# Kernel tuning notes

Measured on AMD Instinct MI355X. Metric: run time of the kernel, lower is better.

The kernel has to match this reference:

```python
import jax, jax.numpy as jnp
import numpy as np

B, N, D, U = 8, 2048, 512, 128


def setup_inputs() -> dict:
    key = jax.random.key(0)
    k_x, k_q, k_k, k_v, k_o = jax.random.split(key, 5)
    scale_in = 1.0 / np.sqrt(D)
    scale_u = 1.0 / np.sqrt(U)
    return {
        "inputs": jax.random.normal(k_x, (B, N, D), dtype=jnp.float32),
        "W_q": jax.random.normal(k_q, (D, U), dtype=jnp.float32) * scale_in,
        "W_k": jax.random.normal(k_k, (D, U), dtype=jnp.float32) * scale_in,
        "W_v": jax.random.normal(k_v, (D, U), dtype=jnp.float32) * scale_in,
        "W_o": jax.random.normal(k_o, (U, D), dtype=jnp.float32) * scale_u,
        "b_o": jnp.zeros((D,), dtype=jnp.float32),
    }


def reference(inputs, W_q, W_k, W_v, W_o, b_o):
    # Single-head scaled dot-product self-attention + output dense + residual
    Q = jnp.einsum('bnd,du->bnu', inputs, W_q)
    K = jnp.einsum('bnd,du->bnu', inputs, W_k)
    V = jnp.einsum('bnd,du->bnu', inputs, W_v)
    inv_sqrt_u = 1.0 / jnp.sqrt(jnp.asarray(W_q.shape[-1], inputs.dtype))
    scores = jnp.einsum('bnu,bmu->bnm', Q, K) * inv_sqrt_u  # [B,N,N]
    attn = jax.nn.softmax(scores, axis=-1)
    ctx = jnp.einsum('bnm,bmu->bnu', attn, V)  # [B,N,U]
    return jnp.einsum('bnu,ud->bnd', ctx, W_o) + b_o + inputs
```

## Files before the change

### kernel.cpp

```cpp
#include <hip/hip_runtime.h>

#define BB 8
#define NN 2048
#define DD 512
#define UU 128
#define SPLITS 8
#define KSPLIT 256
#define TK 32

typedef __bf16 bf16_t;
typedef __bf16 bf16x4 __attribute__((ext_vector_type(4)));
typedef __bf16 bf16x8 __attribute__((ext_vector_type(8)));
typedef float floatx4 __attribute__((ext_vector_type(4)));

__device__ __forceinline__ floatx4 mfma16(bf16x8 a, bf16x8 b, floatx4 c) {
  return __builtin_amdgcn_mfma_f32_16x16x32_bf16(a, b, c, 0, 0, 0);
}

#define SW(r, g) ((((g) ^ ((r) & 7)) * 8))

__device__ __forceinline__ void gld_lds16(const bf16_t* g, bf16_t* l) {
  __builtin_amdgcn_global_load_lds(
      (const __attribute__((address_space(1))) unsigned int*)g,
      (__attribute__((address_space(3))) unsigned int*)l, 16, 0, 0);
}

__global__ __launch_bounds__(256) void cast_x_kernel(const float* __restrict__ x,
                                                     bf16_t* __restrict__ xb) {
  int G = blockIdx.x * 256 + threadIdx.x;
  int token = G >> 6;
  int g = G & 63;
  int dstg = (g & 56) | ((g & 7) ^ (token & 7));
  const float4* src = reinterpret_cast<const float4*>(x) + (size_t)G * 2;
  float4 a = src[0], b = src[1];
  bf16x8 o;
  o[0] = (bf16_t)a.x; o[1] = (bf16_t)a.y; o[2] = (bf16_t)a.z; o[3] = (bf16_t)a.w;
  o[4] = (bf16_t)b.x; o[5] = (bf16_t)b.y; o[6] = (bf16_t)b.z; o[7] = (bf16_t)b.w;
  *reinterpret_cast<bf16x8*>(&xb[(size_t)token * 512 + dstg * 8]) = o;
}

__global__ __launch_bounds__(256) void pack_w_kernel(const float* __restrict__ wq,
                                                     const float* __restrict__ wk,
                                                     const float* __restrict__ wv,
                                                     const float* __restrict__ wo,
                                                     bf16_t* __restrict__ wqkvt,
                                                     bf16_t* __restrict__ wot) {
  int gid = blockIdx.x * 256 + threadIdx.x;
  if (gid < 384 * 512) {
    int nrow = gid >> 9;
    int kdst = gid & 511;
    int ksrc = (kdst & ~56) | (((((kdst >> 3) & 7)) ^ (nrow & 7)) << 3);
    const float* src = (nrow < 128) ? wq : ((nrow < 256) ? wk : wv);
    int n = nrow & 127;
    wqkvt[gid] = (bf16_t)src[ksrc * 128 + n];
  } else {
    int g = gid - 384 * 512;
    int nrow = g >> 7;
    int kdst = g & 127;
    int ksrc = (kdst & ~56) | (((((kdst >> 3) & 7)) ^ (nrow & 7)) << 3);
    wot[g] = (bf16_t)wo[ksrc * 512 + nrow];
  }
}

__global__ __launch_bounds__(256, 2) void qkv_gemm_kernel(const bf16_t* __restrict__ xb,
                                                          const bf16_t* __restrict__ wqkvt,
                                                          bf16_t* __restrict__ Q,
                                                          bf16_t* __restrict__ K,
                                                          bf16_t* __restrict__ Vt) {
  __shared__ bf16_t lA[128 * 64];
  __shared__ bf16_t lB[128 * 64];
  const int m0 = blockIdx.x * 128;
  const int n0 = blockIdx.y * 128;
  const int tid = threadIdx.x;
  const int w = tid >> 6, lane = tid & 63;
  const int quad = lane >> 4, l15 = lane & 15;
  const int mh = (w & 1) * 64, nh = (w >> 1) * 64;

  floatx4 zero4 = {0.f, 0.f, 0.f, 0.f};
  floatx4 acc[4][4];
#pragma unroll
  for (int mt = 0; mt < 4; mt++)
#pragma unroll
    for (int nt = 0; nt < 4; nt++) acc[mt][nt] = zero4;

  for (int kc = 0; kc < 512; kc += 64) {
    __syncthreads();
#pragma unroll
    for (int i = 0; i < 4; i++) {
      int G = tid + i * 256;
      int r = G >> 3, g = G & 7;
      gld_lds16(&xb[(size_t)(m0 + r) * 512 + kc + g * 8], &lA[G * 8]);
    }
#pragma unroll
    for (int i = 0; i < 4; i++) {
      int G = tid + i * 256;
      int r = G >> 3, g = G & 7;
      gld_lds16(&wqkvt[(size_t)(n0 + r) * 512 + kc + g * 8], &lB[G * 8]);
    }
    asm volatile("s_waitcnt vmcnt(0)" ::: "memory");
    __syncthreads();
#pragma unroll
    for (int kb = 0; kb < 2; kb++) {
      bf16x8 af[4], bfr[4];
#pragma unroll
      for (int mt = 0; mt < 4; mt++)
        af[mt] = *reinterpret_cast<const bf16x8*>(
            &lA[(mh + mt * 16 + l15) * 64 + SW(l15, kb * 4 + quad)]);
#pragma unroll
      for (int nt = 0; nt < 4; nt++)
        bfr[nt] = *reinterpret_cast<const bf16x8*>(
            &lB[(nh + nt * 16 + l15) * 64 + SW(l15, kb * 4 + quad)]);
#pragma unroll
      for (int mt = 0; mt < 4; mt++)
#pragma unroll
        for (int nt = 0; nt < 4; nt++)
          acc[mt][nt] = mfma16(af[mt], bfr[nt], acc[mt][nt]);
    }
  }

#pragma unroll
  for (int nt = 0; nt < 4; nt++) {
    int n = n0 + nh + nt * 16 + l15;
#pragma unroll
    for (int mt = 0; mt < 4; mt++) {
#pragma unroll
      for (int r = 0; r < 4; r++) {
        int token = m0 + mh + mt * 16 + quad * 4 + r;
        bf16_t h = (bf16_t)acc[mt][nt][r];
        if (n < 128) {
          Q[(size_t)token * 128 + n] = h;
        } else if (n < 256) {
          int nk = n - 128;
          int nsw = (nk & ~56) | ((((nk >> 3) & 7) ^ (token & 7)) << 3);
          K[(size_t)token * 128 + nsw] = h;
        } else {
          int bb = token >> 11;
          int t = token & 2047;
          int u = n - 256;
          int tsw = (t & ~24) | ((((t >> 3) & 3) ^ (u & 3)) << 3);
          Vt[((size_t)bb * 128 + u) * 2048 + tsw] = h;
        }
      }
    }
  }
}

__global__ __launch_bounds__(256, 3) void attn_kernel(const bf16_t* __restrict__ Q,
                                                      const bf16_t* __restrict__ K,
                                                      const bf16_t* __restrict__ Vt,
                                                      bf16_t* __restrict__ Op,
                                                      float* __restrict__ ml) {
  __shared__ bf16_t lK[2][TK * 128];
  __shared__ bf16_t lV[2][128 * TK];
  __shared__ bf16_t lP[4][32 * TK];

  const int b = blockIdx.y;
  const int qb = blockIdx.x;
  const int s = blockIdx.z;
  const int tid = threadIdx.x;
  const int w = tid >> 6, lane = tid & 63;
  const int quad = lane >> 4, l15 = lane & 15;
  const float c = 0.08838834764831845f * 1.4426950408889634f;

  bf16x8 qf[2][4];
#pragma unroll
  for (int mt = 0; mt < 2; mt++) {
    const bf16_t* qrow =
        &Q[((size_t)b * NN + qb * 128 + w * 32 + mt * 16 + l15) * 128 + quad * 8];
#pragma unroll
    for (int kb = 0; kb < 4; kb++)
      qf[mt][kb] = *reinterpret_cast<const bf16x8*>(qrow + kb * 32);
  }

  float l_part[2] = {0.f, 0.f};
  floatx4 zero4 = {0.f, 0.f, 0.f, 0.f};
  floatx4 accO[2][8];
#pragma unroll
  for (int mt = 0; mt < 2; mt++)
#pragma unroll
    for (int ut = 0; ut < 8; ut++) accO[mt][ut] = zero4;

  bf16_t* pw = &lP[w][0];
  const int kt0 = s * KSPLIT;
  const bf16_t* kbase = &K[((size_t)b * NN + kt0) * 128];
  const bf16_t* vbase = &Vt[(size_t)b * 128 * 2048 + kt0];

  {
#pragma unroll
    for (int i = 0; i < 2; i++) {
      int G = tid + i * 256;
      gld_lds16(kbase + (size_t)G * 8, &lK[0][G * 8]);
    }
#pragma unroll
    for (int i = 0; i < 2; i++) {
      int G = tid + i * 256;
      gld_lds16(vbase + (size_t)(G >> 2) * 2048 + (G & 3) * 8, &lV[0][G * 8]);
    }
  }

  for (int it = 0; it < KSPLIT / TK; it++) {
    const int buf = it & 1;
    if (it < KSPLIT / TK - 1) {
      const int nb = buf ^ 1;
      const bf16_t* ks = kbase + (size_t)(it + 1) * TK * 128;
      const bf16_t* vs = vbase + (it + 1) * TK;
#pragma unroll
      for (int i = 0; i < 2; i++) {
        int G = tid + i * 256;
        gld_lds16(ks + (size_t)G * 8, &lK[nb][G * 8]);
      }
#pragma unroll
      for (int i = 0; i < 2; i++) {
        int G = tid + i * 256;
        gld_lds16(vs + (size_t)(G >> 2) * 2048 + (G & 3) * 8, &lV[nb][G * 8]);
      }
      asm volatile("s_waitcnt vmcnt(4)" ::: "memory");
    } else {
      asm volatile("s_waitcnt vmcnt(0)" ::: "memory");
    }
    asm volatile("s_barrier" ::: "memory");

    floatx4 accS[2][2];
#pragma unroll
    for (int km = 0; km < 2; km++)
#pragma unroll
      for (int mt = 0; mt < 2; mt++) accS[km][mt] = zero4;
#pragma unroll
    for (int kb = 0; kb < 4; kb++) {
#pragma unroll
      for (int km = 0; km < 2; km++) {
        int g = kb * 4 + quad;
        int gs = (g & 8) | ((g & 7) ^ (l15 & 7));
        bf16x8 kf = *reinterpret_cast<const bf16x8*>(
            &lK[buf][(km * 16 + l15) * 128 + gs * 8]);
#pragma unroll
        for (int mt = 0; mt < 2; mt++)
          accS[km][mt] = mfma16(kf, qf[mt][kb], accS[km][mt]);
      }
    }

#pragma unroll
    for (int km = 0; km < 2; km++) {
#pragma unroll
      for (int mt = 0; mt < 2; mt++) {
        float p0 = __builtin_amdgcn_exp2f(accS[km][mt][0] * c);
        float p1 = __builtin_amdgcn_exp2f(accS[km][mt][1] * c);
        float p2 = __builtin_amdgcn_exp2f(accS[km][mt][2] * c);
        float p3 = __builtin_amdgcn_exp2f(accS[km][mt][3] * c);
        l_part[mt] += (p0 + p1) + (p2 + p3);
        bf16x4 pk;
        pk[0] = (bf16_t)p0; pk[1] = (bf16_t)p1; pk[2] = (bf16_t)p2; pk[3] = (bf16_t)p3;
        int q = mt * 16 + l15;
        int gk = (km * 2 + (quad >> 1)) ^ (q & 3);
        *reinterpret_cast<bf16x4*>(&pw[q * TK + gk * 8 + (quad & 1) * 4]) = pk;
      }
    }
    asm volatile("s_waitcnt lgkmcnt(0)" ::: "memory");

    bf16x8 pa[2];
#pragma unroll
    for (int mt = 0; mt < 2; mt++)
      pa[mt] = *reinterpret_cast<const bf16x8*>(
          &pw[(mt * 16 + l15) * TK + (quad ^ (l15 & 3)) * 8]);
#pragma unroll
    for (int ut = 0; ut < 8; ut++) {
      bf16x8 bv = *reinterpret_cast<const bf16x8*>(
          &lV[buf][(ut * 16 + l15) * TK + (quad ^ (l15 & 3)) * 8]);
#pragma unroll
      for (int mt = 0; mt < 2; mt++)
        accO[mt][ut] = mfma16(pa[mt], bv, accO[mt][ut]);
    }
    asm volatile("s_barrier" ::: "memory");
  }

#pragma unroll
  for (int mt = 0; mt < 2; mt++) {
    float v = l_part[mt];
    v += __shfl_xor(v, 16);
    v += __shfl_xor(v, 32);
    l_part[mt] = v;
  }

  size_t base = ((size_t)(b * 16 + qb) * SPLITS + s);
  bf16_t* op = Op + base * (128 * 128);
  float* mlp = ml + base * 128;
#pragma unroll
  for (int mt = 0; mt < 2; mt++)
#pragma unroll
    for (int ut = 0; ut < 8; ut++)
#pragma unroll
      for (int r = 0; r < 4; r++)
        op[(w * 32 + mt * 16 + quad * 4 + r) * 128 + ut * 16 + l15] =
            (bf16_t)accO[mt][ut][r];
  if (quad == 0) {
#pragma unroll
    for (int mt = 0; mt < 2; mt++) mlp[w * 32 + mt * 16 + l15] = l_part[mt];
  }
}

__global__ __launch_bounds__(256) void merge_kernel(const bf16_t* __restrict__ Op,
                                                    const float* __restrict__ ml,
                                                    bf16_t* __restrict__ ctx) {
  const int blk = blockIdx.x;
  const int q = threadIdx.x >> 1;
  const int u0 = blockIdx.y * 64 + (threadIdx.x & 1) * 32;

  float L = 0.f;
  float o[32];
#pragma unroll
  for (int j = 0; j < 32; j++) o[j] = 0.f;
#pragma unroll
  for (int s = 0; s < SPLITS; s++) {
    L += ml[((size_t)blk * SPLITS + s) * 128 + q];
    const bf16_t* op = Op + ((size_t)blk * SPLITS + s) * 16384 + q * 128 + u0;
#pragma unroll
    for (int v = 0; v < 4; v++) {
      bf16x8 ch = *reinterpret_cast<const bf16x8*>(op + v * 8);
#pragma unroll
      for (int j = 0; j < 8; j++) o[v * 8 + j] += (float)ch[j];
    }
  }
  float inv = 1.0f / L;
  const int bb = blk >> 4, qbl = blk & 15;
  bf16_t* dst = ctx + ((size_t)bb * NN + qbl * 128 + q) * 128;
#pragma unroll
  for (int v = 0; v < 4; v++) {
    int g = (u0 >> 3) + v;
    int gsw = (g & 8) | ((g & 7) ^ (q & 7));
    bf16x8 ch;
#pragma unroll
    for (int j = 0; j < 8; j++) ch[j] = (bf16_t)(o[v * 8 + j] * inv);
    *reinterpret_cast<bf16x8*>(dst + gsw * 8) = ch;
  }
}

__global__ __launch_bounds__(256, 4) void out_gemm_kernel(const bf16_t* __restrict__ ctx,
                                                          const bf16_t* __restrict__ wot,
                                                          const float* __restrict__ bo,
                                                          const float* __restrict__ x0,
                                                          float* __restrict__ out) {
  __shared__ bf16_t lA[64 * 128];
  __shared__ bf16_t lB[64 * 128];
  const int m0 = blockIdx.x * 64;
  const int n0 = blockIdx.y * 64;
  const int tid = threadIdx.x;
  const int w = tid >> 6, lane = tid & 63;
  const int quad = lane >> 4, l15 = lane & 15;

#pragma unroll
  for (int i = 0; i < 4; i++) {
    int t = tid + i * 256;
    gld_lds16(&ctx[(size_t)m0 * 128 + t * 8], &lA[t * 8]);
    gld_lds16(&wot[(size_t)n0 * 128 + t * 8], &lB[t * 8]);
  }
  asm volatile("s_waitcnt vmcnt(0)" ::: "memory");
  __syncthreads();

  floatx4 zero4 = {0.f, 0.f, 0.f, 0.f};
  floatx4 acc[4];
#pragma unroll
  for (int nt = 0; nt < 4; nt++) acc[nt] = zero4;
#pragma unroll
  for (int kb = 0; kb < 4; kb++) {
    bf16x8 a = *reinterpret_cast<const bf16x8*>(&lA[(w * 16 + l15) * 128 + SW(l15, kb * 4 + quad)]);
#pragma unroll
    for (int nt = 0; nt < 4; nt++) {
      bf16x8 bfr = *reinterpret_cast<const bf16x8*>(&lB[(nt * 16 + l15) * 128 + SW(l15, kb * 4 + quad)]);
      acc[nt] = mfma16(a, bfr, acc[nt]);
    }
  }

#pragma unroll
  for (int nt = 0; nt < 4; nt++) {
    int n = n0 + nt * 16 + l15;
    float bias = bo[n];
#pragma unroll
    for (int r = 0; r < 4; r++) {
      size_t m = m0 + w * 16 + quad * 4 + r;
      out[m * 512 + n] = acc[nt][r] + bias + x0[m * 512 + n];
    }
  }
}

extern "C" void kernel_launch(void* const* d_in, const int* in_sizes, int n_in,
                              void* d_out, int out_size, void* d_ws, size_t ws_size,
                              hipStream_t stream) {
  const float* x  = (const float*)d_in[0];
  const float* wq = (const float*)d_in[1];
  const float* wk = (const float*)d_in[2];
  const float* wv = (const float*)d_in[3];
  const float* wo = (const float*)d_in[4];
  const float* bo = (const float*)d_in[5];
  float* out = (float*)d_out;

  char* ws = (char*)d_ws;
  bf16_t* Qb    = (bf16_t*)(ws);
  bf16_t* Kb    = (bf16_t*)(ws + 4194304);
  bf16_t* Vt    = (bf16_t*)(ws + 2 * 4194304);
  bf16_t* Ctx   = (bf16_t*)(ws + 3 * 4194304);
  bf16_t* Wqkvt = (bf16_t*)(ws + 4 * 4194304);
  bf16_t* Wot   = (bf16_t*)(ws + 4 * 4194304 + 393216);
  bf16_t* Xb    = (bf16_t*)(ws + 4 * 4194304 + 524288);
  bf16_t* Op    = (bf16_t*)(ws + 4 * 4194304 + 524288);
  float*  ml    = (float*)(ws + 4 * 4194304 + 524288 + 33554432);

  cast_x_kernel<<<4096, 256, 0, stream>>>(x, Xb);
  pack_w_kernel<<<1024, 256, 0, stream>>>(wq, wk, wv, wo, Wqkvt, Wot);
  qkv_gemm_kernel<<<dim3(128, 3), 256, 0, stream>>>(Xb, Wqkvt, Qb, Kb, Vt);
  attn_kernel<<<dim3(16, 8, SPLITS), 256, 0, stream>>>(Qb, Kb, Vt, Op, ml);
  merge_kernel<<<dim3(128, 2), 256, 0, stream>>>(Op, ml, Ctx);
  out_gemm_kernel<<<dim3(256, 8), 256, 0, stream>>>(Ctx, Wot, bo, x, out);
}
```

Baseline: 164.5 us.

## Keep softmax probabilities in registers via transposed 16x16x16 MFMA for PV

The attention kernel no longer round-trips P through shared memory. The S accumulator layout is fed directly as the B operand of a 16x16x16 bf16 MFMA, which computes O transposed, and the epilogue now writes vectorized bf16x4 rows. The key tile grows from 32 to 64 and the double-buffered async prefetch is dropped in favour of a single buffer with sync-load-sync, so global latency is no longer overlapped with compute. The Vt swizzle is widened to 8 groups to match the new 64-wide tile.

```diff
diff --git a/kernel.cpp b/kernel.cpp
--- a/kernel.cpp
+++ b/kernel.cpp
@@ -6,15 +6,20 @@
 #define UU 128
 #define SPLITS 8
 #define KSPLIT 256
-#define TK 32
+#define TK 64
 
 typedef __bf16 bf16_t;
 typedef __bf16 bf16x4 __attribute__((ext_vector_type(4)));
 typedef __bf16 bf16x8 __attribute__((ext_vector_type(8)));
+typedef short s16x4 __attribute__((ext_vector_type(4)));
 typedef float floatx4 __attribute__((ext_vector_type(4)));
 
 __device__ __forceinline__ floatx4 mfma16(bf16x8 a, bf16x8 b, floatx4 c) {
   return __builtin_amdgcn_mfma_f32_16x16x32_bf16(a, b, c, 0, 0, 0);
+}
+__device__ __forceinline__ floatx4 mfma16k16(bf16x4 a, bf16x4 b, floatx4 c) {
+  return __builtin_amdgcn_mfma_f32_16x16x16bf16_1k(
+      __builtin_bit_cast(s16x4, a), __builtin_bit_cast(s16x4, b), c, 0, 0, 0);
 }
 
 #define SW(r, g) ((((g) ^ ((r) & 7)) * 8))
@@ -137,7 +142,7 @@
           int bb = token >> 11;
           int t = token & 2047;
           int u = n - 256;
-          int tsw = (t & ~24) | ((((t >> 3) & 3) ^ (u & 3)) << 3);
+          int tsw = (t & ~56) | ((((t >> 3) & 7) ^ (u & 7)) << 3);
           Vt[((size_t)bb * 128 + u) * 2048 + tsw] = h;
         }
       }
@@ -150,9 +155,8 @@
                                                       const bf16_t* __restrict__ Vt,
                                                       bf16_t* __restrict__ Op,
                                                       float* __restrict__ ml) {
-  __shared__ bf16_t lK[2][TK * 128];
-  __shared__ bf16_t lV[2][128 * TK];
-  __shared__ bf16_t lP[4][32 * TK];
+  __shared__ bf16_t lK[64 * 128];
+  __shared__ bf16_t lV[128 * 64];
 
   const int b = blockIdx.y;
   const int qb = blockIdx.x;
@@ -180,67 +184,49 @@
 #pragma unroll
     for (int ut = 0; ut < 8; ut++) accO[mt][ut] = zero4;
 
-  bf16_t* pw = &lP[w][0];
   const int kt0 = s * KSPLIT;
-  const bf16_t* kbase = &K[((size_t)b * NN + kt0) * 128];
-  const bf16_t* vbase = &Vt[(size_t)b * 128 * 2048 + kt0];
-
-  {
-#pragma unroll
-    for (int i = 0; i < 2; i++) {
-      int G = tid + i * 256;
-      gld_lds16(kbase + (size_t)G * 8, &lK[0][G * 8]);
-    }
-#pragma unroll
-    for (int i = 0; i < 2; i++) {
-      int G = tid + i * 256;
-      gld_lds16(vbase + (size_t)(G >> 2) * 2048 + (G & 3) * 8, &lV[0][G * 8]);
-    }
-  }
-
-  for (int it = 0; it < KSPLIT / TK; it++) {
-    const int buf = it & 1;
-    if (it < KSPLIT / TK - 1) {
-      const int nb = buf ^ 1;
-      const bf16_t* ks = kbase + (size_t)(it + 1) * TK * 128;
-      const bf16_t* vs = vbase + (it + 1) * TK;
-#pragma unroll
-      for (int i = 0; i < 2; i++) {
+  for (int kt = kt0; kt < kt0 + KSPLIT; kt += TK) {
+    __syncthreads();
+    {
+      const bf16_t* ksrc = &K[((size_t)b * NN + kt) * 128];
+#pragma unroll
+      for (int i = 0; i < 4; i++) {
         int G = tid + i * 256;
-        gld_lds16(ks + (size_t)G * 8, &lK[nb][G * 8]);
-      }
-#pragma unroll
-      for (int i = 0; i < 2; i++) {
+        gld_lds16(ksrc + (size_t)G * 8, &lK[G * 8]);
+      }
+      const bf16_t* vsrc = &Vt[(size_t)b * 128 * 2048 + kt];
+#pragma unroll
+      for (int i = 0; i < 4; i++) {
         int G = tid + i * 256;
-        gld_lds16(vs + (size_t)(G >> 2) * 2048 + (G & 3) * 8, &lV[nb][G * 8]);
-      }
-      asm volatile("s_waitcnt vmcnt(4)" ::: "memory");
-    } else {
-      asm volatile("s_waitcnt vmcnt(0)" ::: "memory");
-    }
-    asm volatile("s_barrier" ::: "memory");
-
-    floatx4 accS[2][2];
-#pragma unroll
-    for (int km = 0; km < 2; km++)
+        int u = G >> 3, p = G & 7;
+        gld_lds16(vsrc + (size_t)u * 2048 + p * 8, &lV[G * 8]);
+      }
+    }
+    asm volatile("s_waitcnt vmcnt(0)" ::: "memory");
+    __syncthreads();
+
+    floatx4 accS[4][2];
+#pragma unroll
+    for (int km = 0; km < 4; km++)
 #pragma unroll
       for (int mt = 0; mt < 2; mt++) accS[km][mt] = zero4;
 #pragma unroll
     for (int kb = 0; kb < 4; kb++) {
-#pragma unroll
-      for (int km = 0; km < 2; km++) {
-        int g = kb * 4 + quad;
-        int gs = (g & 8) | ((g & 7) ^ (l15 & 7));
+      int g = kb * 4 + quad;
+      int gs = (g & 8) | ((g & 7) ^ (l15 & 7));
+#pragma unroll
+      for (int km = 0; km < 4; km++) {
         bf16x8 kf = *reinterpret_cast<const bf16x8*>(
-            &lK[buf][(km * 16 + l15) * 128 + gs * 8]);
+            &lK[(km * 16 + l15) * 128 + gs * 8]);
 #pragma unroll
         for (int mt = 0; mt < 2; mt++)
           accS[km][mt] = mfma16(kf, qf[mt][kb], accS[km][mt]);
       }
     }
 
-#pragma unroll
-    for (int km = 0; km < 2; km++) {
+    bf16x4 pb[4][2];
+#pragma unroll
+    for (int km = 0; km < 4; km++) {
 #pragma unroll
       for (int mt = 0; mt < 2; mt++) {
         float p0 = __builtin_amdgcn_exp2f(accS[km][mt][0] * c);
@@ -250,27 +236,23 @@
         l_part[mt] += (p0 + p1) + (p2 + p3);
         bf16x4 pk;
         pk[0] = (bf16_t)p0; pk[1] = (bf16_t)p1; pk[2] = (bf16_t)p2; pk[3] = (bf16_t)p3;
-        int q = mt * 16 + l15;
-        int gk = (km * 2 + (quad >> 1)) ^ (q & 3);
-        *reinterpret_cast<bf16x4*>(&pw[q * TK + gk * 8 + (quad & 1) * 4]) = pk;
-      }
-    }
-    asm volatile("s_waitcnt lgkmcnt(0)" ::: "memory");
-
-    bf16x8 pa[2];
-#pragma unroll
-    for (int mt = 0; mt < 2; mt++)
-      pa[mt] = *reinterpret_cast<const bf16x8*>(
-          &pw[(mt * 16 + l15) * TK + (quad ^ (l15 & 3)) * 8]);
-#pragma unroll
-    for (int ut = 0; ut < 8; ut++) {
-      bf16x8 bv = *reinterpret_cast<const bf16x8*>(
-          &lV[buf][(ut * 16 + l15) * TK + (quad ^ (l15 & 3)) * 8]);
-#pragma unroll
-      for (int mt = 0; mt < 2; mt++)
-        accO[mt][ut] = mfma16(pa[mt], bv, accO[mt][ut]);
-    }
-    asm volatile("s_barrier" ::: "memory");
+        pb[km][mt] = pk;
+      }
+    }
+
+#pragma unroll
+    for (int km = 0; km < 4; km++) {
+      int g16 = (km * 2 + (quad >> 1)) ^ (l15 & 7);
+      int off = g16 * 8 + (quad & 1) * 4;
+#pragma unroll
+      for (int ut = 0; ut < 8; ut++) {
+        bf16x4 va = *reinterpret_cast<const bf16x4*>(
+            &lV[(ut * 16 + l15) * 64 + off]);
+#pragma unroll
+        for (int mt = 0; mt < 2; mt++)
+          accO[mt][ut] = mfma16k16(va, pb[km][mt], accO[mt][ut]);
+      }
+    }
   }
 
 #pragma unroll
@@ -285,13 +267,16 @@
   bf16_t* op = Op + base * (128 * 128);
   float* mlp = ml + base * 128;
 #pragma unroll
-  for (int mt = 0; mt < 2; mt++)
-#pragma unroll
-    for (int ut = 0; ut < 8; ut++)
-#pragma unroll
-      for (int r = 0; r < 4; r++)
-        op[(w * 32 + mt * 16 + quad * 4 + r) * 128 + ut * 16 + l15] =
-            (bf16_t)accO[mt][ut][r];
+  for (int mt = 0; mt < 2; mt++) {
+#pragma unroll
+    for (int ut = 0; ut < 8; ut++) {
+      bf16x4 ov;
+#pragma unroll
+      for (int r = 0; r < 4; r++) ov[r] = (bf16_t)accO[mt][ut][r];
+      *reinterpret_cast<bf16x4*>(
+          &op[(w * 32 + mt * 16 + l15) * 128 + ut * 16 + quad * 4]) = ov;
+    }
+  }
   if (quad == 0) {
 #pragma unroll
     for (int mt = 0; mt < 2; mt++) mlp[w * 32 + mt * 16 + l15] = l_part[mt];
```

New measurement: 166.4 us. About the same (+1.2%).
